# Performance work log

Hardware: AMD Instinct MI355X
Metric: run time of the kernel (lower is better)

The kernel has to match this reference:

```python
import jax, jax.numpy as jnp
import numpy as np

# alpha_r0 = exp(i * z) with z = 1j  ->  exp(-1), stored as complex64 buffer in torch
ALPHA = jnp.complex64(np.exp(1j * 1j))
NUM_ITERS = 15


def _apply_r0(v, alpha):
    """Bidirectional first-order IIR filter. v: (B, N) complex64.
    fwd[t] = v[t] + alpha*fwd[t-1];  bwd[t] = v[t] + alpha*bwd[t+1].
    Returns (i/2) * (fwd + bwd - v)."""
    vT = v.T  # (N, B) -- scan over time axis
    init = jnp.zeros(v.shape[0], dtype=v.dtype)

    def step(c, vt):
        c = vt + alpha * c
        return c, c

    _, fwd = jax.lax.scan(step, init, vT)
    _, bwd = jax.lax.scan(step, init, vT, reverse=True)
    return 0.5j * (fwd.T + bwd.T - v)


def _normalize(x):
    # F.normalize(dim=1) for complex: divide by max(l2 norm, 1e-12)
    n = jnp.sqrt(jnp.sum(jnp.abs(x) ** 2, axis=-1, keepdims=True))
    return x / jnp.maximum(n, 1e-12)


def _power_iteration(v_magnitude, num_iters=NUM_ITERS):
    B, N = v_magnitude.shape
    # torch: torch.sqrt(v + 1e-9).to(complex64) -- real sqrt, then cast
    D = jnp.sqrt(v_magnitude + 1e-9).astype(jnp.complex64)
    kr, ki = jax.random.split(jax.random.key(42))
    b_k = (jax.random.normal(kr, (B, N)) + 1j * jax.random.normal(ki, (B, N))).astype(jnp.complex64)
    b_k = _normalize(b_k)

    def body(b, _):
        w = D * _apply_r0(D * b, ALPHA)
        return _normalize(w), None

    b_k, _ = jax.lax.scan(body, b_k, None, length=num_iters)
    w = D * _apply_r0(D * b_k, ALPHA)
    eigenvalue = jnp.sum(jnp.conj(b_k) * w, axis=-1)  # (B,)
    return eigenvalue, b_k


def setup_inputs() -> dict:
    key = jax.random.key(0)
    k1, k2, k3, k4, k5 = jax.random.split(key, 5)
    B, N, V, D = 2, 2048, 32000, 1024
    prediction = jax.random.normal(k1, (B, N, V), dtype=jnp.float32)
    target = jax.random.randint(k2, (B, N), 0, V)
    hidden_states = jax.random.normal(k3, (B, N, D), dtype=jnp.float32)
    W1 = jax.random.normal(k4, (D, D // 2), dtype=jnp.float32) * (1.0 / np.sqrt(D))
    b1 = jnp.zeros((D // 2,), dtype=jnp.float32)
    W2 = jax.random.normal(k5, (D // 2, 1), dtype=jnp.float32) * (1.0 / np.sqrt(D // 2))
    b2 = jnp.zeros((1,), dtype=jnp.float32)
    return {"prediction": prediction, "target": target, "hidden_states": hidden_states,
            "W1": W1, "b1": b1, "W2": W2, "b2": b2}


def reference(prediction, target, hidden_states, W1, b1, W2, b2):
    # error magnitude from softmax prob of the target token
    pred_probs = jax.nn.softmax(prediction, axis=-1)           # (B, N, V)
    target_probs = jnp.take_along_axis(pred_probs, target[..., None], axis=-1)[..., 0]
    error_mag = 1.0 - target_probs                             # (B, N)

    # decay_function: Linear -> Tanh -> Linear -> Softplus
    h = jnp.tanh(hidden_states @ W1 + b1)                      # (B, N, D/2)
    sigma = jax.nn.softplus(h @ W2 + b2)[..., 0]               # (B, N)

    v_magnitude = error_mag * sigma
    dom_eig, _ = _power_iteration(v_magnitude, NUM_ITERS)

    eig_phase = jnp.angle(dom_eig)
    interference = jnp.abs(dom_eig.imag)
    resonance_score = interference * jnp.cos(eig_phase)
    dissonance_score = interference * jnp.abs(eig_phase - jnp.pi) / jnp.pi
    return resonance_score, dissonance_score, dom_eig
```

## Files before the change

### kernel.cpp

```cpp
#include <hip/hip_runtime.h>
#include <cstdint>
#include <cstddef>

#define NROWS 4096
#define VDIM  32000
#define NDIM  2048
#define KDIM  1024
#define CDIM  512
#define KTAPS 16

__device__ __forceinline__ uint32_t rotl32(uint32_t v, int r){ return (v<<r)|(v>>(32-r)); }

__device__ __forceinline__ void threefry2x32(uint32_t k0, uint32_t k1, uint32_t c0, uint32_t c1,
                                             uint32_t& o0, uint32_t& o1){
  uint32_t ks2 = k0 ^ k1 ^ 0x1BD11BDAu;
  uint32_t x0 = c0 + k0, x1 = c1 + k1;
  x0+=x1; x1=rotl32(x1,13); x1^=x0;
  x0+=x1; x1=rotl32(x1,15); x1^=x0;
  x0+=x1; x1=rotl32(x1,26); x1^=x0;
  x0+=x1; x1=rotl32(x1, 6); x1^=x0;
  x0+=k1; x1+=ks2+1u;
  x0+=x1; x1=rotl32(x1,17); x1^=x0;
  x0+=x1; x1=rotl32(x1,29); x1^=x0;
  x0+=x1; x1=rotl32(x1,16); x1^=x0;
  x0+=x1; x1=rotl32(x1,24); x1^=x0;
  x0+=ks2; x1+=k0+2u;
  x0+=x1; x1=rotl32(x1,13); x1^=x0;
  x0+=x1; x1=rotl32(x1,15); x1^=x0;
  x0+=x1; x1=rotl32(x1,26); x1^=x0;
  x0+=x1; x1=rotl32(x1, 6); x1^=x0;
  x0+=k0; x1+=k1+3u;
  x0+=x1; x1=rotl32(x1,17); x1^=x0;
  x0+=x1; x1=rotl32(x1,29); x1^=x0;
  x0+=x1; x1=rotl32(x1,16); x1^=x0;
  x0+=x1; x1=rotl32(x1,24); x1^=x0;
  x0+=k1; x1+=ks2+4u;
  x0+=x1; x1=rotl32(x1,13); x1^=x0;
  x0+=x1; x1=rotl32(x1,15); x1^=x0;
  x0+=x1; x1=rotl32(x1,26); x1^=x0;
  x0+=x1; x1=rotl32(x1, 6); x1^=x0;
  x0+=ks2; x1+=k0+5u;
  o0=x0; o1=x1;
}

__device__ __forceinline__ float erfinvf_xla(float x){
  float w = -log1pf(-x*x);
  float p;
  if (w < 5.0f){
    w -= 2.5f;
    p =  2.81022636e-08f;
    p = fmaf(p,w, 3.43273939e-07f);
    p = fmaf(p,w,-3.5233877e-06f);
    p = fmaf(p,w,-4.39150654e-06f);
    p = fmaf(p,w, 0.00021858087f);
    p = fmaf(p,w,-0.00125372503f);
    p = fmaf(p,w,-0.00417768164f);
    p = fmaf(p,w, 0.246640727f);
    p = fmaf(p,w, 1.50140941f);
  } else {
    w = sqrtf(w) - 3.0f;
    p = -0.000200214257f;
    p = fmaf(p,w, 0.000100950558f);
    p = fmaf(p,w, 0.00134934322f);
    p = fmaf(p,w,-0.00367342844f);
    p = fmaf(p,w, 0.00573950773f);
    p = fmaf(p,w,-0.0076224613f);
    p = fmaf(p,w, 0.00943887047f);
    p = fmaf(p,w, 1.00167406f);
    p = fmaf(p,w, 2.83297682f);
  }
  return p*x;
}

__device__ __forceinline__ float bits_to_uniform(uint32_t bits){
  float u = __uint_as_float((bits >> 9) | 0x3f800000u) - 1.0f;
  float v = fmaf(u, 2.0f, -0.99999994f);
  return fmaxf(-0.99999994f, v);
}

__global__ __launch_bounds__(256) void softmax_err_kernel(const float* __restrict__ pred,
                                                          const int* __restrict__ target,
                                                          float* __restrict__ err){
  const int r = blockIdx.x;
  const int tid = threadIdx.x;
  const float* row = pred + (size_t)r * VDIM;
  float m = -3.4e38f, s = 0.0f;
  for (int i = tid*4; i < VDIM; i += 1024){
    float4 x = *(const float4*)(row + i);
    float mx = fmaxf(fmaxf(x.x, x.y), fmaxf(x.z, x.w));
    if (mx > m){ s *= expf(m - mx); m = mx; }
    s += expf(x.x - m) + expf(x.y - m) + expf(x.z - m) + expf(x.w - m);
  }
  #pragma unroll
  for (int o = 32; o > 0; o >>= 1){
    float m2 = __shfl_xor(m, o);
    float s2 = __shfl_xor(s, o);
    float M = fmaxf(m, m2);
    s = s*expf(m - M) + s2*expf(m2 - M);
    m = M;
  }
  __shared__ float lm[4], ls[4];
  if ((tid & 63) == 0){ lm[tid>>6] = m; ls[tid>>6] = s; }
  __syncthreads();
  if (tid == 0){
    float M = lm[0], S = ls[0];
    #pragma unroll
    for (int w = 1; w < 4; w++){
      float M2 = fmaxf(M, lm[w]);
      S = S*expf(M - M2) + ls[w]*expf(lm[w] - M2);
      M = M2;
    }
    float t = row[target[r]];
    err[r] = 1.0f - expf(t - M) / S;
  }
}

__global__ __launch_bounds__(256) void gemm_tanh_kernel(const float* __restrict__ A,
                                                        const float* __restrict__ B,
                                                        const float* __restrict__ b1,
                                                        const float* __restrict__ W2,
                                                        float* __restrict__ part){
  const int mb = blockIdx.x;
  const int nb = blockIdx.y;
  __shared__ float As[16][64];
  __shared__ float Bs[16][64];
  const int tid = threadIdx.x;
  const int tx = tid & 15, ty = tid >> 4;
  float acc[4][4] = {{0.f}};

  for (int k0 = 0; k0 < KDIM; k0 += 16){
    {
      int m  = tid >> 2, kq = tid & 3;
      float4 a = *(const float4*)(A + (size_t)(mb*64 + m)*KDIM + k0 + kq*4);
      As[kq*4+0][m] = a.x; As[kq*4+1][m] = a.y; As[kq*4+2][m] = a.z; As[kq*4+3][m] = a.w;
      int kk = tid >> 4, n4 = tid & 15;
      float4 b = *(const float4*)(B + (size_t)(k0 + kk)*CDIM + nb*64 + n4*4);
      *(float4*)&Bs[kk][n4*4] = b;
    }
    __syncthreads();
    #pragma unroll
    for (int k = 0; k < 16; k++){
      float4 av = *(float4*)&As[k][ty*4];
      float4 bv = *(float4*)&Bs[k][tx*4];
      float aa[4] = {av.x, av.y, av.z, av.w};
      float bb[4] = {bv.x, bv.y, bv.z, bv.w};
      #pragma unroll
      for (int i = 0; i < 4; i++)
        #pragma unroll
        for (int j = 0; j < 4; j++)
          acc[i][j] = fmaf(aa[i], bb[j], acc[i][j]);
    }
    __syncthreads();
  }

  __shared__ float red[64][16];
  #pragma unroll
  for (int i = 0; i < 4; i++){
    float s = 0.f;
    #pragma unroll
    for (int j = 0; j < 4; j++){
      int n = nb*64 + tx*4 + j;
      float h = tanhf(acc[i][j] + b1[n]);
      s = fmaf(h, W2[n], s);
    }
    red[ty*4+i][tx] = s;
  }
  __syncthreads();
  if (tid < 64){
    float s = 0.f;
    #pragma unroll
    for (int t = 0; t < 16; t++) s += red[tid][t];
    part[(size_t)(mb*64 + tid)*8 + nb] = s;
  }
}

__device__ __forceinline__ float blockReduce1024(float v, float* red){
  #pragma unroll
  for (int o = 32; o > 0; o >>= 1) v += __shfl_down(v, o);
  __syncthreads();
  if ((threadIdx.x & 63) == 0) red[threadIdx.x >> 6] = v;
  __syncthreads();
  float s = 0.f;
  #pragma unroll
  for (int i = 0; i < 16; i++) s += red[i];
  return s;
}

__global__ __launch_bounds__(1024) void power_iter_kernel(const float* __restrict__ part,
                                                          const float* __restrict__ err,
                                                          const float* __restrict__ b2,
                                                          float* __restrict__ out,
                                                          int out_size){
  const int b = blockIdx.x;
  const int tid = threadIdx.x;
  __shared__ __align__(16) float sDv[NDIM];
  __shared__ __align__(16) float sbr[NDIM], sbi[NDIM];
  __shared__ __align__(16) float svr[NDIM + 2*KTAPS], svi[NDIM + 2*KTAPS];
  __shared__ float red[16];

  float coef[KTAPS+1];
  {
    double a = (double)0.36787944117144233f;
    double p = 1.0;
    #pragma unroll
    for (int k = 0; k <= KTAPS; k++){ coef[k] = (float)p; p *= a; }
  }

  uint32_t kr0, kr1, ki0, ki1;
  threefry2x32(0u, 42u, 0u, 0u, kr0, kr1);
  threefry2x32(0u, 42u, 0u, 1u, ki0, ki1);

  const float b2v = b2[0];
  float nrm_local = 0.f;
  for (int n = tid; n < NDIM; n += 1024){
    int i = b*NDIM + n;
    float s = 0.f;
    #pragma unroll
    for (int j = 0; j < 8; j++) s += part[(size_t)i*8 + j];
    s += b2v;
    float sp = fmaxf(s, 0.f) + log1pf(expf(-fabsf(s)));
    sDv[n] = sqrtf(err[i]*sp + 1e-9f);

    uint32_t r0, r1, q0, q1;
    threefry2x32(kr0, kr1, 0u, (uint32_t)i, r0, r1);
    threefry2x32(ki0, ki1, 0u, (uint32_t)i, q0, q1);
    uint32_t rb = r0 ^ r1;
    uint32_t ib = q0 ^ q1;
    float br = 1.41421356f * erfinvf_xla(bits_to_uniform(rb));
    float bi = 1.41421356f * erfinvf_xla(bits_to_uniform(ib));
    sbr[n] = br; sbi[n] = bi;
    nrm_local += br*br + bi*bi;
  }
  {
    float nrm = blockReduce1024(nrm_local, red);
    float scale = 1.0f / fmaxf(sqrtf(nrm), 1e-12f);
    for (int n = tid; n < NDIM; n += 1024){ sbr[n] *= scale; sbi[n] *= scale; }
    __syncthreads();
  }

  for (int it = 0; it < 16; ++it){
    const bool fin = (it == 15);
    for (int idx = tid; idx < NDIM + 2*KTAPS; idx += 1024){
      int i = idx - KTAPS;
      bool in = (i >= 0) && (i < NDIM);
      float d  = in ? sDv[i] : 0.f;
      svr[idx] = in ? d * sbr[i] : 0.f;
      svi[idx] = in ? d * sbi[i] : 0.f;
    }
    __syncthreads();

    float la = 0.f, lb = 0.f;
    if (tid < 512){
      const int t0 = tid * 4;
      float sr4[4], si4[4];
      {
        float win[36];
        #pragma unroll
        for (int j = 0; j < 9; j++){
          float4 x = *(float4*)&svr[t0 + 4*j];
          win[4*j] = x.x; win[4*j+1] = x.y; win[4*j+2] = x.z; win[4*j+3] = x.w;
        }
        #pragma unroll
        for (int m = 0; m < 4; m++){
          float s = win[m + KTAPS];
          #pragma unroll
          for (int k = 1; k <= KTAPS; k++) s = fmaf(coef[k], win[m+KTAPS-k] + win[m+KTAPS+k], s);
          sr4[m] = s;
        }
      }
      {
        float win[36];
        #pragma unroll
        for (int j = 0; j < 9; j++){
          float4 x = *(float4*)&svi[t0 + 4*j];
          win[4*j] = x.x; win[4*j+1] = x.y; win[4*j+2] = x.z; win[4*j+3] = x.w;
        }
        #pragma unroll
        for (int m = 0; m < 4; m++){
          float s = win[m + KTAPS];
          #pragma unroll
          for (int k = 1; k <= KTAPS; k++) s = fmaf(coef[k], win[m+KTAPS-k] + win[m+KTAPS+k], s);
          si4[m] = s;
        }
      }
      #pragma unroll
      for (int m = 0; m < 4; m++){
        float d  = sDv[t0 + m];
        float wr = -0.5f * d * si4[m];
        float wi =  0.5f * d * sr4[m];
        if (!fin){
          sbr[t0+m] = wr; sbi[t0+m] = wi;
          la += wr*wr + wi*wi;
        } else {
          la += sbr[t0+m]*wr + sbi[t0+m]*wi;
          lb += sbr[t0+m]*wi - sbi[t0+m]*wr;
        }
      }
    }
    if (!fin){
      float nrm = blockReduce1024(la, red);
      float scale = 1.0f / fmaxf(sqrtf(nrm), 1e-12f);
      for (int n = tid; n < NDIM; n += 1024){ sbr[n] *= scale; sbi[n] *= scale; }
      __syncthreads();
    } else {
      float er = blockReduce1024(la, red);
      float ei = blockReduce1024(lb, red);
      if (tid == 0){
        const float PI = 3.14159274f;
        float phase = atan2f(ei, er);
        float intf  = fabsf(ei);
        out[b]     = intf * cosf(phase);
        out[2 + b] = intf * fabsf(phase - PI) / PI;
        if (out_size >= 8){
          out[4 + b] = er;
          out[6 + b] = ei;
        } else {
          out[4 + b] = er;
        }
      }
    }
  }
}

extern "C" void kernel_launch(void* const* d_in, const int* in_sizes, int n_in,
                              void* d_out, int out_size, void* d_ws, size_t ws_size,
                              hipStream_t stream){
  (void)in_sizes; (void)n_in; (void)ws_size;
  const float* pred   = (const float*)d_in[0];
  const int*   target = (const int*)  d_in[1];
  const float* hs     = (const float*)d_in[2];
  const float* W1     = (const float*)d_in[3];
  const float* b1     = (const float*)d_in[4];
  const float* W2     = (const float*)d_in[5];
  const float* b2     = (const float*)d_in[6];
  float* out  = (float*)d_out;
  float* err  = (float*)d_ws;
  float* part = err + NROWS;

  softmax_err_kernel<<<NROWS, 256, 0, stream>>>(pred, target, err);
  gemm_tanh_kernel<<<dim3(NROWS/64, CDIM/64), 256, 0, stream>>>(hs, W1, b1, W2, part);
  power_iter_kernel<<<2, 1024, 0, stream>>>(part, err, b2, out, out_size);
}
```

Measured before the change: 829.4 us.

## Fuse softmax and GEMM kernels into one launch, split power-iteration channels across threads

Merges the softmax-error and GEMM-tanh kernels into a single grid: the GEMM tiles come first and the softmax rows after, so both run concurrently and one launch is saved. The softmax uses exp2f with a log2e prescale. In the power iteration, real and imaginary stencils are spread over all 1024 threads instead of 512. The explicit normalization pass is replaced by folding the scale into the next iteration's input and the final eigenvalue. Risks are slight numerical differences from exp2f and from the deferred scaling, plus shared-memory aliasing in the fused kernel.

After: 730.4 us. 11.9% less time.

```diff
diff --git a/kernel.cpp b/kernel.cpp
--- a/kernel.cpp
+++ b/kernel.cpp
@@ -8,6 +8,9 @@
 #define KDIM  1024
 #define CDIM  512
 #define KTAPS 16
+
+#define GEMM_BLOCKS 512
+#define FUSED_GRID  (GEMM_BLOCKS + NROWS)
 
 __device__ __forceinline__ uint32_t rotl32(uint32_t v, int r){ return (v<<r)|(v>>(32-r)); }
 
@@ -78,99 +81,104 @@
   return fmaxf(-0.99999994f, v);
 }
 
-__global__ __launch_bounds__(256) void softmax_err_kernel(const float* __restrict__ pred,
-                                                          const int* __restrict__ target,
-                                                          float* __restrict__ err){
-  const int r = blockIdx.x;
+__global__ __launch_bounds__(256) void fused_sm_gemm(const float* __restrict__ pred,
+                                                     const int* __restrict__ target,
+                                                     const float* __restrict__ A,
+                                                     const float* __restrict__ B,
+                                                     const float* __restrict__ b1,
+                                                     const float* __restrict__ W2,
+                                                     float* __restrict__ err,
+                                                     float* __restrict__ part){
+  __shared__ float smem[3072];
   const int tid = threadIdx.x;
-  const float* row = pred + (size_t)r * VDIM;
-  float m = -3.4e38f, s = 0.0f;
-  for (int i = tid*4; i < VDIM; i += 1024){
-    float4 x = *(const float4*)(row + i);
-    float mx = fmaxf(fmaxf(x.x, x.y), fmaxf(x.z, x.w));
-    if (mx > m){ s *= expf(m - mx); m = mx; }
-    s += expf(x.x - m) + expf(x.y - m) + expf(x.z - m) + expf(x.w - m);
-  }
-  #pragma unroll
-  for (int o = 32; o > 0; o >>= 1){
-    float m2 = __shfl_xor(m, o);
-    float s2 = __shfl_xor(s, o);
-    float M = fmaxf(m, m2);
-    s = s*expf(m - M) + s2*expf(m2 - M);
-    m = M;
-  }
-  __shared__ float lm[4], ls[4];
-  if ((tid & 63) == 0){ lm[tid>>6] = m; ls[tid>>6] = s; }
-  __syncthreads();
-  if (tid == 0){
-    float M = lm[0], S = ls[0];
+
+  if (blockIdx.x < GEMM_BLOCKS){
+    const int mb = blockIdx.x >> 3;
+    const int nb = blockIdx.x & 7;
+    float (*As)[64] = reinterpret_cast<float(*)[64]>(smem);
+    float (*Bs)[64] = reinterpret_cast<float(*)[64]>(smem + 1024);
+    const int tx = tid & 15, ty = tid >> 4;
+    float acc[4][4] = {{0.f}};
+
+    for (int k0 = 0; k0 < KDIM; k0 += 16){
+      {
+        int m  = tid >> 2, kq = tid & 3;
+        float4 a = *(const float4*)(A + (size_t)(mb*64 + m)*KDIM + k0 + kq*4);
+        As[kq*4+0][m] = a.x; As[kq*4+1][m] = a.y; As[kq*4+2][m] = a.z; As[kq*4+3][m] = a.w;
+        int kk = tid >> 4, n4 = tid & 15;
+        float4 bv = *(const float4*)(B + (size_t)(k0 + kk)*CDIM + nb*64 + n4*4);
+        *(float4*)&Bs[kk][n4*4] = bv;
+      }
+      __syncthreads();
+      #pragma unroll
+      for (int k = 0; k < 16; k++){
+        float4 av = *(float4*)&As[k][ty*4];
+        float4 bv = *(float4*)&Bs[k][tx*4];
+        float aa[4] = {av.x, av.y, av.z, av.w};
+        float bb[4] = {bv.x, bv.y, bv.z, bv.w};
+        #pragma unroll
+        for (int i = 0; i < 4; i++)
+          #pragma unroll
+          for (int j = 0; j < 4; j++)
+            acc[i][j] = fmaf(aa[i], bb[j], acc[i][j]);
+      }
+      __syncthreads();
+    }
+
+    float (*red)[16] = reinterpret_cast<float(*)[16]>(smem + 2048);
     #pragma unroll
-    for (int w = 1; w < 4; w++){
-      float M2 = fmaxf(M, lm[w]);
-      S = S*expf(M - M2) + ls[w]*expf(lm[w] - M2);
-      M = M2;
-    }
-    float t = row[target[r]];
-    err[r] = 1.0f - expf(t - M) / S;
-  }
-}
-
-__global__ __launch_bounds__(256) void gemm_tanh_kernel(const float* __restrict__ A,
-                                                        const float* __restrict__ B,
-                                                        const float* __restrict__ b1,
-                                                        const float* __restrict__ W2,
-                                                        float* __restrict__ part){
-  const int mb = blockIdx.x;
-  const int nb = blockIdx.y;
-  __shared__ float As[16][64];
-  __shared__ float Bs[16][64];
-  const int tid = threadIdx.x;
-  const int tx = tid & 15, ty = tid >> 4;
-  float acc[4][4] = {{0.f}};
-
-  for (int k0 = 0; k0 < KDIM; k0 += 16){
-    {
-      int m  = tid >> 2, kq = tid & 3;
-      float4 a = *(const float4*)(A + (size_t)(mb*64 + m)*KDIM + k0 + kq*4);
-      As[kq*4+0][m] = a.x; As[kq*4+1][m] = a.y; As[kq*4+2][m] = a.z; As[kq*4+3][m] = a.w;
-      int kk = tid >> 4, n4 = tid & 15;
-      float4 b = *(const float4*)(B + (size_t)(k0 + kk)*CDIM + nb*64 + n4*4);
-      *(float4*)&Bs[kk][n4*4] = b;
+    for (int i = 0; i < 4; i++){
+      float s = 0.f;
+      #pragma unroll
+      for (int j = 0; j < 4; j++){
+        int n = nb*64 + tx*4 + j;
+        float h = tanhf(acc[i][j] + b1[n]);
+        s = fmaf(h, W2[n], s);
+      }
+      red[ty*4+i][tx] = s;
     }
     __syncthreads();
+    if (tid < 64){
+      float s = 0.f;
+      #pragma unroll
+      for (int t = 0; t < 16; t++) s += red[tid][t];
+      part[(size_t)(mb*64 + tid)*8 + nb] = s;
+    }
+  } else {
+    const int r = blockIdx.x - GEMM_BLOCKS;
+    const float* row = pred + (size_t)r * VDIM;
+    const float L2E = 1.44269504f;
+    float m = -3.4e38f, s = 0.0f;
+    for (int i = tid*4; i < VDIM; i += 1024){
+      float4 x = *(const float4*)(row + i);
+      float mx = fmaxf(fmaxf(x.x, x.y), fmaxf(x.z, x.w));
+      if (mx > m){ s *= exp2f((m - mx)*L2E); m = mx; }
+      s += exp2f((x.x - m)*L2E) + exp2f((x.y - m)*L2E)
+         + exp2f((x.z - m)*L2E) + exp2f((x.w - m)*L2E);
+    }
     #pragma unroll
-    for (int k = 0; k < 16; k++){
-      float4 av = *(float4*)&As[k][ty*4];
-      float4 bv = *(float4*)&Bs[k][tx*4];
-      float aa[4] = {av.x, av.y, av.z, av.w};
-      float bb[4] = {bv.x, bv.y, bv.z, bv.w};
-      #pragma unroll
-      for (int i = 0; i < 4; i++)
-        #pragma unroll
-        for (int j = 0; j < 4; j++)
-          acc[i][j] = fmaf(aa[i], bb[j], acc[i][j]);
-    }
+    for (int o = 32; o > 0; o >>= 1){
+      float m2 = __shfl_xor(m, o);
+      float s2 = __shfl_xor(s, o);
+      float M = fmaxf(m, m2);
+      s = s*exp2f((m - M)*L2E) + s2*exp2f((m2 - M)*L2E);
+      m = M;
+    }
+    float* lm = smem;
+    float* ls = smem + 8;
+    if ((tid & 63) == 0){ lm[tid>>6] = m; ls[tid>>6] = s; }
     __syncthreads();
-  }
-
-  __shared__ float red[64][16];
-  #pragma unroll
-  for (int i = 0; i < 4; i++){
-    float s = 0.f;
-    #pragma unroll
-    for (int j = 0; j < 4; j++){
-      int n = nb*64 + tx*4 + j;
-      float h = tanhf(acc[i][j] + b1[n]);
-      s = fmaf(h, W2[n], s);
-    }
-    red[ty*4+i][tx] = s;
-  }
-  __syncthreads();
-  if (tid < 64){
-    float s = 0.f;
-    #pragma unroll
-    for (int t = 0; t < 16; t++) s += red[tid][t];
-    part[(size_t)(mb*64 + tid)*8 + nb] = s;
+    if (tid == 0){
+      float M = lm[0], S = ls[0];
+      #pragma unroll
+      for (int w = 1; w < 4; w++){
+        float M2 = fmaxf(M, lm[w]);
+        S = S*exp2f((M - M2)*L2E) + ls[w]*exp2f((lm[w] - M2)*L2E);
+        M = M2;
+      }
+      float t = row[target[r]];
+      err[r] = 1.0f - exp2f((t - M)*L2E) / S;
+    }
   }
 }
 
@@ -231,93 +239,85 @@
     sbr[n] = br; sbi[n] = bi;
     nrm_local += br*br + bi*bi;
   }
+  float scale;
   {
     float nrm = blockReduce1024(nrm_local, red);
-    float scale = 1.0f / fmaxf(sqrtf(nrm), 1e-12f);
-    for (int n = tid; n < NDIM; n += 1024){ sbr[n] *= scale; sbi[n] *= scale; }
-    __syncthreads();
-  }
-
+    scale = 1.0f / fmaxf(sqrtf(nrm), 1e-12f);
+  }
+
+  float er = 0.f, ei = 0.f;
   for (int it = 0; it < 16; ++it){
     const bool fin = (it == 15);
     for (int idx = tid; idx < NDIM + 2*KTAPS; idx += 1024){
       int i = idx - KTAPS;
       bool in = (i >= 0) && (i < NDIM);
-      float d  = in ? sDv[i] : 0.f;
-      svr[idx] = in ? d * sbr[i] : 0.f;
-      svi[idx] = in ? d * sbi[i] : 0.f;
+      float ds = in ? sDv[i] * scale : 0.f;
+      svr[idx] = in ? ds * sbr[i] : 0.f;
+      svi[idx] = in ? ds * sbi[i] : 0.f;
     }
     __syncthreads();
 
     float la = 0.f, lb = 0.f;
-    if (tid < 512){
-      const int t0 = tid * 4;
-      float sr4[4], si4[4];
-      {
-        float win[36];
+    {
+      const int ch = tid >> 9;
+      const int t0 = (tid & 511) * 4;
+      const float* __restrict__ src = ch ? svi : svr;
+      float win[36];
+      #pragma unroll
+      for (int j = 0; j < 9; j++){
+        float4 x = *(const float4*)&src[t0 + 4*j];
+        win[4*j] = x.x; win[4*j+1] = x.y; win[4*j+2] = x.z; win[4*j+3] = x.w;
+      }
+      float s4[4];
+      #pragma unroll
+      for (int m = 0; m < 4; m++){
+        float s = win[m + KTAPS];
         #pragma unroll
-        for (int j = 0; j < 9; j++){
-          float4 x = *(float4*)&svr[t0 + 4*j];
-          win[4*j] = x.x; win[4*j+1] = x.y; win[4*j+2] = x.z; win[4*j+3] = x.w;
-        }
+        for (int k = 1; k <= KTAPS; k++) s = fmaf(coef[k], win[m+KTAPS-k] + win[m+KTAPS+k], s);
+        s4[m] = s;
+      }
+      if (ch == 0){
         #pragma unroll
         for (int m = 0; m < 4; m++){
-          float s = win[m + KTAPS];
-          #pragma unroll
-          for (int k = 1; k <= KTAPS; k++) s = fmaf(coef[k], win[m+KTAPS-k] + win[m+KTAPS+k], s);
-          sr4[m] = s;
+          float d  = sDv[t0 + m];
+          float wi = 0.5f * d * s4[m];
+          if (!fin){ sbi[t0+m] = wi; la += wi*wi; }
+          else     { la += sbi[t0+m]*wi;
+                     lb += sbr[t0+m]*wi; }
         }
-      }
-      {
-        float win[36];
-        #pragma unroll
-        for (int j = 0; j < 9; j++){
-          float4 x = *(float4*)&svi[t0 + 4*j];
-          win[4*j] = x.x; win[4*j+1] = x.y; win[4*j+2] = x.z; win[4*j+3] = x.w;
-        }
+      } else {
         #pragma unroll
         for (int m = 0; m < 4; m++){
-          float s = win[m + KTAPS];
-          #pragma unroll
-          for (int k = 1; k <= KTAPS; k++) s = fmaf(coef[k], win[m+KTAPS-k] + win[m+KTAPS+k], s);
-          si4[m] = s;
-        }
-      }
-      #pragma unroll
-      for (int m = 0; m < 4; m++){
-        float d  = sDv[t0 + m];
-        float wr = -0.5f * d * si4[m];
-        float wi =  0.5f * d * sr4[m];
-        if (!fin){
-          sbr[t0+m] = wr; sbi[t0+m] = wi;
-          la += wr*wr + wi*wi;
-        } else {
-          la += sbr[t0+m]*wr + sbi[t0+m]*wi;
-          lb += sbr[t0+m]*wi - sbi[t0+m]*wr;
+          float d  = sDv[t0 + m];
+          float wr = -0.5f * d * s4[m];
+          if (!fin){ sbr[t0+m] = wr; la += wr*wr; }
+          else     { la += sbr[t0+m]*wr;
+                     lb -= sbi[t0+m]*wr; }
         }
       }
     }
     if (!fin){
       float nrm = blockReduce1024(la, red);
-      float scale = 1.0f / fmaxf(sqrtf(nrm), 1e-12f);
-      for (int n = tid; n < NDIM; n += 1024){ sbr[n] *= scale; sbi[n] *= scale; }
-      __syncthreads();
+      scale = 1.0f / fmaxf(sqrtf(nrm), 1e-12f);
     } else {
-      float er = blockReduce1024(la, red);
-      float ei = blockReduce1024(lb, red);
-      if (tid == 0){
-        const float PI = 3.14159274f;
-        float phase = atan2f(ei, er);
-        float intf  = fabsf(ei);
-        out[b]     = intf * cosf(phase);
-        out[2 + b] = intf * fabsf(phase - PI) / PI;
-        if (out_size >= 8){
-          out[4 + b] = er;
-          out[6 + b] = ei;
-        } else {
-          out[4 + b] = er;
-        }
-      }
+      float s_er = blockReduce1024(la, red);
+      float s_ei = blockReduce1024(lb, red);
+      er = s_er * scale;
+      ei = s_ei * scale;
+    }
+  }
+
+  if (tid == 0){
+    const float PI = 3.14159274f;
+    float phase = atan2f(ei, er);
+    float intf  = fabsf(ei);
+    out[b]     = intf * cosf(phase);
+    out[2 + b] = intf * fabsf(phase - PI) / PI;
+    if (out_size >= 8){
+      out[4 + b] = er;
+      out[6 + b] = ei;
+    } else {
+      out[4 + b] = er;
     }
   }
 }
@@ -337,7 +337,6 @@
   float* err  = (float*)d_ws;
   float* part = err + NROWS;
 
-  softmax_err_kernel<<<NROWS, 256, 0, stream>>>(pred, target, err);
-  gemm_tanh_kernel<<<dim3(NROWS/64, CDIM/64), 256, 0, stream>>>(hs, W1, b1, W2, part);
+  fused_sm_gemm<<<FUSED_GRID, 256, 0, stream>>>(pred, target, hs, W1, b1, W2, err, part);
   power_iter_kernel<<<2, 1024, 0, stream>>>(part, err, b2, out, out_size);
 }
```
